# Kernel tuning notes

Measured on AMD Instinct MI355X. Metric: run time of the kernel, lower is better.

## Reference

```python
import jax, jax.numpy as jnp
import numpy as np

B, N, D = 4, 4096, 1024
DFF = 4 * D
K = 2048  # max(1, int(N * 0.5))


def setup_inputs() -> dict:
    key = jax.random.key(0)
    ks = jax.random.split(key, 4)
    x = jax.random.normal(ks[0], (B, N, D), dtype=jnp.float32)
    gate_w = jax.random.normal(ks[1], (1, D), dtype=jnp.float32) * 0.02
    w1 = jax.random.normal(ks[2], (D, DFF), dtype=jnp.float32) * (1.0 / np.sqrt(D))
    b1 = jnp.zeros((DFF,), dtype=jnp.float32)
    w2 = jax.random.normal(ks[3], (DFF, D), dtype=jnp.float32) * (1.0 / np.sqrt(DFF))
    b2 = jnp.zeros((D,), dtype=jnp.float32)
    return {"x": x, "gate_w": gate_w, "w1": w1, "b1": b1, "w2": w2, "b2": b2, "k": K}


def reference(x, gate_w, w1, b1, w2, b2, k):
    # scores: [B, N] = gate(x).squeeze(-1)
    scores = jnp.einsum("bnd,d->bn", x, gate_w[0])
    _, topk = jax.lax.top_k(scores, k)          # [B, k] token indices
    # gather selected tokens: [B, k, D]
    x_sel = jnp.take_along_axis(x, topk[:, :, None], axis=1)
    # ffn (d -> 4d -> d, GELU) + residual on selected tokens only
    h = jax.nn.gelu(x_sel @ w1 + b1) @ w2 + b2
    x_proc = x_sel + h
    # scatter processed tokens back into a copy of x
    b_idx = jnp.arange(x.shape[0])[:, None]      # [B, 1]
    out = x.at[b_idx, topk].set(x_proc)
    return out
```

## Files before the change

### kernel.cpp

```cpp
#include <hip/hip_runtime.h>
#include <math.h>

#define B_   4
#define N_   4096
#define D_   1024
#define DFF_ 4096
#define K_   2048

typedef __attribute__((ext_vector_type(8))) short short8;
typedef __attribute__((ext_vector_type(4))) float float4v;

__device__ __forceinline__ unsigned short f2bf(float f) {
    unsigned int u = __float_as_uint(f);
    u = (u + 0x7fffu + ((u >> 16) & 1u)) >> 16;
    return (unsigned short)u;
}

__device__ __forceinline__ void gld16(const void* g, void* l) {
    __builtin_amdgcn_global_load_lds((const __attribute__((address_space(1))) void*)g,
                                     (__attribute__((address_space(3))) void*)l, 16, 0, 0);
}

__global__ __launch_bounds__(256) void scores_kernel(const float* __restrict__ x,
                                                     const float* __restrict__ gate_w,
                                                     float* __restrict__ scores,
                                                     int* __restrict__ slot) {
    int wave = (blockIdx.x * blockDim.x + threadIdx.x) >> 6;
    int lane = threadIdx.x & 63;
    if (wave >= B_ * N_) return;
    if (lane == 1) slot[wave] = -1;
    const float4* xr = (const float4*)(x + (size_t)wave * D_);
    const float4* g  = (const float4*)gate_w;
    float acc = 0.f;
    #pragma unroll
    for (int j = 0; j < D_ / 4 / 64; ++j) {
        float4 a = xr[lane + j * 64];
        float4 b = g[lane + j * 64];
        acc += a.x * b.x + a.y * b.y + a.z * b.z + a.w * b.w;
    }
    #pragma unroll
    for (int off = 32; off > 0; off >>= 1) acc += __shfl_down(acc, off, 64);
    if (lane == 0) scores[wave] = acc;
}

__global__ __launch_bounds__(1024) void select_topk_kernel(const float* __restrict__ scores,
                                                           int* __restrict__ topk,
                                                           int* __restrict__ slot) {
    __shared__ unsigned key[N_];
    __shared__ unsigned hist[256];
    __shared__ int sh_bin, sh_rem, sh_ngt;
    __shared__ int wsum[16], woff[16];
    int b = blockIdx.x, tid = threadIdx.x;
    int lane = tid & 63, wid = tid >> 6;

    for (int i = tid; i < N_; i += 1024) {
        unsigned u = __float_as_uint(scores[b * N_ + i]);
        key[i] = (u & 0x80000000u) ? ~u : (u | 0x80000000u);
    }
    if (tid == 0) sh_ngt = 0;
    __syncthreads();

    unsigned prefix = 0, pmask = 0;
    int rem = K_;
    for (int shift = 24; shift >= 0; shift -= 8) {
        if (tid < 256) hist[tid] = 0;
        __syncthreads();
        for (int i = tid; i < N_; i += 1024) {
            unsigned k = key[i];
            if ((k & pmask) == prefix) atomicAdd(&hist[(k >> shift) & 255u], 1u);
        }
        __syncthreads();
        if (tid < 64) {
            unsigned v0 = hist[4 * lane], v1 = hist[4 * lane + 1];
            unsigned v2 = hist[4 * lane + 2], v3 = hist[4 * lane + 3];
            unsigned s3 = v3, s2 = v2 + s3, s1 = v1 + s2, s0 = v0 + s1;
            unsigned t = s0;
            #pragma unroll
            for (int off = 1; off < 64; off <<= 1) {
                unsigned u = __shfl_down(t, off, 64);
                if (lane + off < 64) t += u;
            }
            unsigned above = t - s0;
            unsigned S0 = s0 + above, S1 = s1 + above, S2 = s2 + above, S3 = s3 + above;
            unsigned R = (unsigned)rem;
            if (S0 >= R && S1 < R) { sh_bin = 4 * lane;     sh_rem = rem - (int)S1; }
            if (S1 >= R && S2 < R) { sh_bin = 4 * lane + 1; sh_rem = rem - (int)S2; }
            if (S2 >= R && S3 < R) { sh_bin = 4 * lane + 2; sh_rem = rem - (int)S3; }
            if (S3 >= R && above < R) { sh_bin = 4 * lane + 3; sh_rem = rem - (int)above; }
        }
        __syncthreads();
        prefix |= ((unsigned)sh_bin) << shift;
        pmask  |= 0xffu << shift;
        rem = sh_rem;
    }
    unsigned T = prefix;
    int c_gt = K_ - rem;

    for (int i = tid; i < N_; i += 1024) {
        bool p = key[i] > T;
        unsigned long long m = __ballot(p);
        int cnt = __popcll(m);
        int basepos = 0;
        if (lane == 0 && cnt) basepos = atomicAdd(&sh_ngt, cnt);
        basepos = __shfl(basepos, 0, 64);
        if (p) {
            int pos = basepos + __popcll(m & ((1ULL << lane) - 1ULL));
            topk[b * K_ + pos] = i;
            slot[b * N_ + i] = b * K_ + pos;
        }
    }
    int base = tid * 4, c = 0;
    #pragma unroll
    for (int j = 0; j < 4; ++j) c += (key[base + j] == T);
    int sc = c;
    #pragma unroll
    for (int off = 1; off < 64; off <<= 1) {
        int u = __shfl_up(sc, off, 64);
        if (lane >= off) sc += u;
    }
    if (lane == 63) wsum[wid] = sc;
    __syncthreads();
    if (tid == 0) {
        int run = 0;
        #pragma unroll
        for (int j = 0; j < 16; ++j) { woff[j] = run; run += wsum[j]; }
    }
    __syncthreads();
    int r = woff[wid] + sc - c;
    #pragma unroll
    for (int j = 0; j < 4; ++j) {
        if (key[base + j] == T) {
            if (r < rem) {
                topk[b * K_ + c_gt + r] = base + j;
                slot[b * N_ + base + j] = b * K_ + c_gt + r;
            }
            ++r;
        }
    }
}

__global__ __launch_bounds__(256) void gather_copy_kernel(const float* __restrict__ x,
                                                          const int* __restrict__ slot,
                                                          unsigned short* __restrict__ xsel,
                                                          float* __restrict__ out) {
    int row = blockIdx.x;
    int t = threadIdx.x;
    int s = slot[row];
    float4 v = ((const float4*)(x + (size_t)row * D_))[t];
    if (s >= 0) {
        ushort4 o;
        o.x = f2bf(v.x); o.y = f2bf(v.y); o.z = f2bf(v.z); o.w = f2bf(v.w);
        ((ushort4*)(xsel + (size_t)s * D_))[t] = o;
    } else {
        ((float4*)(out + (size_t)row * D_))[t] = v;
    }
}

__global__ __launch_bounds__(256) void transpose_both_kernel(const float* __restrict__ w1,
                                                             const float* __restrict__ w2,
                                                             unsigned short* __restrict__ w1t,
                                                             unsigned short* __restrict__ w2t) {
    __shared__ float tile[32][33];
    int bid = blockIdx.x;
    const float* src; unsigned short* dst; int R, C, bx, by;
    if (bid < 4096) { src = w1; dst = w1t; R = D_;   C = DFF_; bx = bid & 127;          by = bid >> 7; }
    else            { src = w2; dst = w2t; R = DFF_; C = D_;   bx = (bid - 4096) & 31;  by = (bid - 4096) >> 5; }
    int tx = threadIdx.x & 31, ty = threadIdx.x >> 5;
    int c = bx * 32 + tx, r0 = by * 32;
    #pragma unroll
    for (int j = ty; j < 32; j += 8) tile[j][tx] = src[(size_t)(r0 + j) * C + c];
    __syncthreads();
    int dc = by * 32 + tx, dr0 = bx * 32;
    #pragma unroll
    for (int j = ty; j < 32; j += 8) dst[(size_t)(dr0 + j) * R + dc] = f2bf(tile[tx][j]);
}


__global__ __launch_bounds__(512, 2) void ffn1_pipe_kernel(const unsigned short* __restrict__ A,
                                                           const unsigned short* __restrict__ Bt,
                                                           const float* __restrict__ b1,
                                                           unsigned short* __restrict__ h1) {
    constexpr int K  = D_;
    constexpr int NT = K / 32;
    __shared__ __align__(16) unsigned short smem[65536];

    const int t    = threadIdx.x;
    const int lane = t & 63;
    const int wid  = t >> 6;
    const int quad = lane >> 4;
    const int lr   = lane & 15;
    const int wr   = wid >> 2;
    const int wc   = wid & 3;
    const int row0 = blockIdx.x * 256;
    const int col0 = blockIdx.y * 256;

    const int ch0 = t, ch1 = t + 512;
    const int rp0 = ch0 >> 3, w0 = (ch0 & 7) ^ (rp0 & 7);
    const int rp1 = ch1 >> 3, w1 = (ch1 & 7) ^ (rp1 & 7);
    const int gr0 = rp0 * 2 + (w0 >> 2), gc0 = w0 & 3;
    const int gr1 = rp1 * 2 + (w1 >> 2), gc1 = w1 & 3;
    const char* aS0 = (const char*)A  + ((size_t)(row0 + gr0) * K + (size_t)gc0 * 8) * 2;
    const char* aS1 = (const char*)A  + ((size_t)(row0 + gr1) * K + (size_t)gc1 * 8) * 2;
    const char* bS0 = (const char*)Bt + ((size_t)(col0 + gr0) * K + (size_t)gc0 * 8) * 2;
    const char* bS1 = (const char*)Bt + ((size_t)(col0 + gr1) * K + (size_t)gc1 * 8) * 2;
    const int oA0 = ch0 * 8, oA1 = ch1 * 8;
    const int oB0 = 8192 + ch0 * 8, oB1 = 8192 + ch1 * 8;

    const int rbA = wr * 128 + lr, rA2 = rbA >> 1;
    const int aoff = (rA2 * 8 + ((((rbA & 1) << 2) | quad) ^ (rA2 & 7))) * 8;
    const int rbB = wc * 64 + lr, rB2 = rbB >> 1;
    const int boff = 8192 + (rB2 * 8 + ((((rbB & 1) << 2) | quad) ^ (rB2 & 7))) * 8;

    #pragma unroll
    for (int pt = 0; pt < 3; ++pt) {
        unsigned short* buf = smem + pt * 16384;
        gld16(aS0, buf + oA0); gld16(aS1, buf + oA1);
        gld16(bS0, buf + oB0); gld16(bS1, buf + oB1);
        aS0 += 64; aS1 += 64; bS0 += 64; bS1 += 64;
    }
    asm volatile("s_waitcnt vmcnt(8)" ::: "memory");
    __builtin_amdgcn_s_barrier();

    float4v acc[8][4] = {};
    short8 af[8], bq[4];

    #pragma unroll 4
    for (int kt = 0; kt < NT; ++kt) {
        unsigned short* cur = smem + (kt & 3) * 16384;
        unsigned short* nxt = smem + ((kt + 3) & 3) * 16384;
        const bool pf = (kt + 3 < NT);

        #pragma unroll
        for (int mi = 0; mi < 4; ++mi) af[mi] = *(const short8*)(cur + aoff + mi * 512);
        #pragma unroll
        for (int ni = 0; ni < 4; ++ni) bq[ni] = *(const short8*)(cur + boff + ni * 512);
        if (pf) { gld16(aS0, nxt + oA0); gld16(aS1, nxt + oA1); }
        __builtin_amdgcn_s_barrier();
        __builtin_amdgcn_s_setprio(1);
        #pragma unroll
        for (int mi = 0; mi < 4; ++mi)
            #pragma unroll
            for (int ni = 0; ni < 4; ++ni)
                acc[mi][ni] = __builtin_amdgcn_mfma_f32_16x16x32_bf16(af[mi], bq[ni], acc[mi][ni], 0, 0, 0);
        __builtin_amdgcn_s_setprio(0);
        __builtin_amdgcn_s_barrier();

        #pragma unroll
        for (int mi = 4; mi < 8; ++mi) af[mi] = *(const short8*)(cur + aoff + mi * 512);
        if (pf) { gld16(bS0, nxt + oB0); gld16(bS1, nxt + oB1); }
        aS0 += 64; aS1 += 64; bS0 += 64; bS1 += 64;
        if (kt < NT - 3)       asm volatile("s_waitcnt vmcnt(8)" ::: "memory");
        else if (kt == NT - 3) asm volatile("s_waitcnt vmcnt(4)" ::: "memory");
        else                   asm volatile("s_waitcnt vmcnt(0)" ::: "memory");
        __builtin_amdgcn_s_barrier();
        __builtin_amdgcn_s_setprio(1);
        #pragma unroll
        for (int mi = 4; mi < 8; ++mi)
            #pragma unroll
            for (int ni = 0; ni < 4; ++ni)
                acc[mi][ni] = __builtin_amdgcn_mfma_f32_16x16x32_bf16(af[mi], bq[ni], acc[mi][ni], 0, 0, 0);
        __builtin_amdgcn_s_setprio(0);
        __builtin_amdgcn_s_barrier();
    }

    float bias[4];
    #pragma unroll
    for (int ni = 0; ni < 4; ++ni) bias[ni] = b1[col0 + wc * 64 + ni * 16 + lr];
    unsigned short* ws_ = smem + wid * 5120;
    const int ro = row0 + wr * 128;
    const int co = col0 + wc * 64;
    #pragma unroll
    for (int p = 0; p < 2; ++p) {
        #pragma unroll
        for (int mi = 0; mi < 8; ++mi)
            #pragma unroll
            for (int nj = 0; nj < 2; ++nj) {
                const int ni = p * 2 + nj;
                #pragma unroll
                for (int r = 0; r < 4; ++r) {
                    float u = acc[mi][ni][r] + bias[ni];
                    float tt = 1.5957691216057308f * u * (1.0f + 0.044715f * u * u);
                    float g = u / (1.0f + __expf(-tt));
                    ws_[(mi * 16 + quad * 4 + r) * 40 + nj * 16 + lr] = f2bf(g);
                }
            }
        asm volatile("s_waitcnt lgkmcnt(0)" ::: "memory");
        #pragma unroll
        for (int j = 0; j < 8; ++j) {
            const int chk = lane + j * 64;
            const int rr = chk >> 2, cc = chk & 3;
            short8 v = *(const short8*)(ws_ + rr * 40 + cc * 8);
            *(short8*)(h1 + (size_t)(ro + rr) * DFF_ + co + p * 32 + cc * 8) = v;
        }
        asm volatile("s_waitcnt lgkmcnt(0)" ::: "memory");
    }
}

__global__ __launch_bounds__(512, 2) void ffn2_pipe_kernel(const unsigned short* __restrict__ A,
                                                           const unsigned short* __restrict__ Bt,
                                                           const float* __restrict__ b2,
                                                           const float* __restrict__ x,
                                                           const int* __restrict__ topk,
                                                           float* __restrict__ out) {
    constexpr int K  = DFF_;
    constexpr int NT = K / 32;
    __shared__ __align__(16) unsigned short smem[49152];

    const int t    = threadIdx.x;
    const int lane = t & 63;
    const int wid  = t >> 6;
    const int quad = lane >> 4;
    const int lr   = lane & 15;
    const int wr   = wid >> 2;
    const int wc   = wid & 3;
    const int row0 = blockIdx.x * 128;
    const int col0 = blockIdx.y * 256;

    const int chA = t;
    const int rpa = chA >> 3, wa = (chA & 7) ^ (rpa & 7);
    const char* aS = (const char*)A + ((size_t)(row0 + rpa * 2 + (wa >> 2)) * K + (size_t)(wa & 3) * 8) * 2;
    const int ch0 = t, ch1 = t + 512;
    const int rp0 = ch0 >> 3, w0 = (ch0 & 7) ^ (rp0 & 7);
    const int rp1 = ch1 >> 3, w1 = (ch1 & 7) ^ (rp1 & 7);
    const char* bS0 = (const char*)Bt + ((size_t)(col0 + rp0 * 2 + (w0 >> 2)) * K + (size_t)(w0 & 3) * 8) * 2;
    const char* bS1 = (const char*)Bt + ((size_t)(col0 + rp1 * 2 + (w1 >> 2)) * K + (size_t)(w1 & 3) * 8) * 2;
    const int oA = chA * 8;
    const int oB0 = 4096 + ch0 * 8, oB1 = 4096 + ch1 * 8;

    const int rbA = wr * 64 + lr, rA2 = rbA >> 1;
    const int aoff = (rA2 * 8 + ((((rbA & 1) << 2) | quad) ^ (rA2 & 7))) * 8;
    const int rbB = wc * 64 + lr, rB2 = rbB >> 1;
    const int boff = 4096 + (rB2 * 8 + ((((rbB & 1) << 2) | quad) ^ (rB2 & 7))) * 8;

    #pragma unroll
    for (int pt = 0; pt < 3; ++pt) {
        unsigned short* buf = smem + pt * 12288;
        gld16(aS, buf + oA); gld16(bS0, buf + oB0); gld16(bS1, buf + oB1);
        aS += 64; bS0 += 64; bS1 += 64;
    }
    asm volatile("s_waitcnt vmcnt(6)" ::: "memory");
    __builtin_amdgcn_s_barrier();

    float4v acc[4][4] = {};
    short8 af[4], bq[4];

    #pragma unroll 4
    for (int kt = 0; kt < NT; ++kt) {
        unsigned short* cur = smem + (kt & 3) * 12288;
        unsigned short* nxt = smem + ((kt + 3) & 3) * 12288;
        const bool pf = (kt + 3 < NT);

        af[0] = *(const short8*)(cur + aoff);
        af[1] = *(const short8*)(cur + aoff + 512);
        #pragma unroll
        for (int ni = 0; ni < 4; ++ni) bq[ni] = *(const short8*)(cur + boff + ni * 512);
        if (pf) { gld16(aS, nxt + oA); gld16(bS0, nxt + oB0); }
        __builtin_amdgcn_s_barrier();
        __builtin_amdgcn_s_setprio(1);
        #pragma unroll
        for (int mi = 0; mi < 2; ++mi)
            #pragma unroll
            for (int ni = 0; ni < 4; ++ni)
                acc[mi][ni] = __builtin_amdgcn_mfma_f32_16x16x32_bf16(af[mi], bq[ni], acc[mi][ni], 0, 0, 0);
        __builtin_amdgcn_s_setprio(0);
        __builtin_amdgcn_s_barrier();

        af[2] = *(const short8*)(cur + aoff + 1024);
        af[3] = *(const short8*)(cur + aoff + 1536);
        if (pf) { gld16(bS1, nxt + oB1); }
        aS += 64; bS0 += 64; bS1 += 64;
        if (kt < NT - 3)       asm volatile("s_waitcnt vmcnt(6)" ::: "memory");
        else if (kt == NT - 3) asm volatile("s_waitcnt vmcnt(3)" ::: "memory");
        else                   asm volatile("s_waitcnt vmcnt(0)" ::: "memory");
        __builtin_amdgcn_s_barrier();
        __builtin_amdgcn_s_setprio(1);
        #pragma unroll
        for (int mi = 2; mi < 4; ++mi)
            #pragma unroll
            for (int ni = 0; ni < 4; ++ni)
                acc[mi][ni] = __builtin_amdgcn_mfma_f32_16x16x32_bf16(af[mi], bq[ni], acc[mi][ni], 0, 0, 0);
        __builtin_amdgcn_s_setprio(0);
        __builtin_amdgcn_s_barrier();
    }

    #pragma unroll
    for (int mi = 0; mi < 4; ++mi) {
        #pragma unroll
        for (int r = 0; r < 4; ++r) {
            int row = row0 + wr * 64 + mi * 16 + quad * 4 + r;
            int gb = row >> 11;
            int tok = topk[row];
            size_t base = ((size_t)(gb * N_ + tok)) * D_;
            #pragma unroll
            for (int ni = 0; ni < 4; ++ni) {
                int col = col0 + wc * 64 + ni * 16 + lr;
                out[base + col] = x[base + col] + acc[mi][ni][r] + b2[col];
            }
        }
    }
}

extern "C" void kernel_launch(void* const* d_in, const int* in_sizes, int n_in,
                              void* d_out, int out_size, void* d_ws, size_t ws_size,
                              hipStream_t stream) {
    const float* x      = (const float*)d_in[0];
    const float* gate_w = (const float*)d_in[1];
    const float* w1     = (const float*)d_in[2];
    const float* b1     = (const float*)d_in[3];
    const float* w2     = (const float*)d_in[4];
    const float* b2     = (const float*)d_in[5];
    float* out = (float*)d_out;

    char* ws = (char*)d_ws;
    float*          scores = (float*)ws;
    int*            topk   = (int*)(ws + (64 << 10));
    int*            slot   = (int*)(ws + (96 << 10));
    unsigned short* xsel   = (unsigned short*)(ws + (160 << 10));
    unsigned short* w1t    = (unsigned short*)(ws + (160 << 10) + (16 << 20));
    unsigned short* w2t    = (unsigned short*)(ws + (160 << 10) + (24 << 20));
    unsigned short* h1     = (unsigned short*)(ws + (160 << 10) + (32 << 20));

    scores_kernel<<<(B_ * N_) / 4, 256, 0, stream>>>(x, gate_w, scores, slot);
    select_topk_kernel<<<B_, 1024, 0, stream>>>(scores, topk, slot);

    transpose_both_kernel<<<8192, 256, 0, stream>>>(w1, w2, w1t, w2t);

    gather_copy_kernel<<<B_ * N_, 256, 0, stream>>>(x, slot, xsel, out);

    ffn1_pipe_kernel<<<dim3(32, 16), 512, 0, stream>>>(xsel, w1t, b1, h1);
    ffn2_pipe_kernel<<<dim3(64, 4), 512, 0, stream>>>(h1, w2t, b2, x, topk, out);
}
```

Measured before the change: 335.4 us.

## Replace 4-stage LDS pipelines with smaller-tile double-buffered GEMM kernels

Both FFN GEMMs move from a 4-buffer, 3-deep prefetch pipeline with large block tiles to a simple two-buffer ping-pong scheme with smaller tiles. FFN1 goes from 256x256 to 256x128 tiles (more blocks, 4 blocks/CU bound), and FFN2 from 128x256 with 512 threads to 128x128 with 256 threads. The goal is higher occupancy and more blocks in flight, with less LDS per block, to hide latency. The cost is a full vmcnt(0) wait every k-step, which exposes global load latency, plus lower data reuse per tile.

```diff
diff --git a/kernel.cpp b/kernel.cpp
--- a/kernel.cpp
+++ b/kernel.cpp
@@ -176,66 +176,59 @@
 }
 
 
-__global__ __launch_bounds__(512, 2) void ffn1_pipe_kernel(const unsigned short* __restrict__ A,
-                                                           const unsigned short* __restrict__ Bt,
-                                                           const float* __restrict__ b1,
-                                                           unsigned short* __restrict__ h1) {
+__global__ __launch_bounds__(512, 4) void ffn1_db_kernel(const unsigned short* __restrict__ A,
+                                                         const unsigned short* __restrict__ Bt,
+                                                         const float* __restrict__ b1,
+                                                         unsigned short* __restrict__ h1) {
     constexpr int K  = D_;
     constexpr int NT = K / 32;
-    __shared__ __align__(16) unsigned short smem[65536];
+    __shared__ __align__(16) unsigned short smem[24576];
 
     const int t    = threadIdx.x;
     const int lane = t & 63;
     const int wid  = t >> 6;
     const int quad = lane >> 4;
     const int lr   = lane & 15;
-    const int wr   = wid >> 2;
-    const int wc   = wid & 3;
+    const int wr   = wid >> 1;
+    const int wc   = wid & 1;
     const int row0 = blockIdx.x * 256;
-    const int col0 = blockIdx.y * 256;
-
-    const int ch0 = t, ch1 = t + 512;
-    const int rp0 = ch0 >> 3, w0 = (ch0 & 7) ^ (rp0 & 7);
-    const int rp1 = ch1 >> 3, w1 = (ch1 & 7) ^ (rp1 & 7);
-    const int gr0 = rp0 * 2 + (w0 >> 2), gc0 = w0 & 3;
-    const int gr1 = rp1 * 2 + (w1 >> 2), gc1 = w1 & 3;
-    const char* aS0 = (const char*)A  + ((size_t)(row0 + gr0) * K + (size_t)gc0 * 8) * 2;
-    const char* aS1 = (const char*)A  + ((size_t)(row0 + gr1) * K + (size_t)gc1 * 8) * 2;
-    const char* bS0 = (const char*)Bt + ((size_t)(col0 + gr0) * K + (size_t)gc0 * 8) * 2;
-    const char* bS1 = (const char*)Bt + ((size_t)(col0 + gr1) * K + (size_t)gc1 * 8) * 2;
-    const int oA0 = ch0 * 8, oA1 = ch1 * 8;
-    const int oB0 = 8192 + ch0 * 8, oB1 = 8192 + ch1 * 8;
-
-    const int rbA = wr * 128 + lr, rA2 = rbA >> 1;
+    const int col0 = blockIdx.y * 128;
+
+    const int chA0 = t, chA1 = t + 512, chB = t;
+    const int rpA0 = chA0 >> 3, wA0 = (chA0 & 7) ^ (rpA0 & 7);
+    const int rpA1 = chA1 >> 3, wA1 = (chA1 & 7) ^ (rpA1 & 7);
+    const int rpB  = chB  >> 3, wB  = (chB  & 7) ^ (rpB  & 7);
+    const char* aS0 = (const char*)A  + ((size_t)(row0 + rpA0 * 2 + (wA0 >> 2)) * K + (size_t)(wA0 & 3) * 8) * 2;
+    const char* aS1 = (const char*)A  + ((size_t)(row0 + rpA1 * 2 + (wA1 >> 2)) * K + (size_t)(wA1 & 3) * 8) * 2;
+    const char* bS  = (const char*)Bt + ((size_t)(col0 + rpB  * 2 + (wB  >> 2)) * K + (size_t)(wB  & 3) * 8) * 2;
+    const int oA0 = chA0 * 8, oA1 = chA1 * 8, oB = 8192 + chB * 8;
+
+    const int rbA = wr * 64 + lr, rA2 = rbA >> 1;
     const int aoff = (rA2 * 8 + ((((rbA & 1) << 2) | quad) ^ (rA2 & 7))) * 8;
     const int rbB = wc * 64 + lr, rB2 = rbB >> 1;
     const int boff = 8192 + (rB2 * 8 + ((((rbB & 1) << 2) | quad) ^ (rB2 & 7))) * 8;
 
-    #pragma unroll
-    for (int pt = 0; pt < 3; ++pt) {
-        unsigned short* buf = smem + pt * 16384;
-        gld16(aS0, buf + oA0); gld16(aS1, buf + oA1);
-        gld16(bS0, buf + oB0); gld16(bS1, buf + oB1);
-        aS0 += 64; aS1 += 64; bS0 += 64; bS1 += 64;
-    }
-    asm volatile("s_waitcnt vmcnt(8)" ::: "memory");
+    unsigned short* lds0 = smem;
+    unsigned short* lds1 = smem + 12288;
+
+    gld16(aS0, lds0 + oA0); gld16(aS1, lds0 + oA1); gld16(bS, lds0 + oB);
+    aS0 += 64; aS1 += 64; bS += 64;
+    asm volatile("s_waitcnt vmcnt(0)" ::: "memory");
     __builtin_amdgcn_s_barrier();
 
-    float4v acc[8][4] = {};
-    short8 af[8], bq[4];
-
-    #pragma unroll 4
-    for (int kt = 0; kt < NT; ++kt) {
-        unsigned short* cur = smem + (kt & 3) * 16384;
-        unsigned short* nxt = smem + ((kt + 3) & 3) * 16384;
-        const bool pf = (kt + 3 < NT);
-
+    float4v acc[4][4] = {};
+    short8 af[4], bq[4];
+
+    auto step = [&](const unsigned short* cur, unsigned short* nxt, bool pf) {
         #pragma unroll
         for (int mi = 0; mi < 4; ++mi) af[mi] = *(const short8*)(cur + aoff + mi * 512);
         #pragma unroll
         for (int ni = 0; ni < 4; ++ni) bq[ni] = *(const short8*)(cur + boff + ni * 512);
-        if (pf) { gld16(aS0, nxt + oA0); gld16(aS1, nxt + oA1); }
-        __builtin_amdgcn_s_barrier();
+        if (pf) {
+            gld16(aS0, nxt + oA0); gld16(aS1, nxt + oA1); gld16(bS, nxt + oB);
+            aS0 += 64; aS1 += 64; bS += 64;
+        }
+        __builtin_amdgcn_sched_barrier(0);
         __builtin_amdgcn_s_setprio(1);
         #pragma unroll
         for (int mi = 0; mi < 4; ++mi)
@@ -243,88 +236,70 @@
             for (int ni = 0; ni < 4; ++ni)
                 acc[mi][ni] = __builtin_amdgcn_mfma_f32_16x16x32_bf16(af[mi], bq[ni], acc[mi][ni], 0, 0, 0);
         __builtin_amdgcn_s_setprio(0);
+        asm volatile("s_waitcnt vmcnt(0)" ::: "memory");
         __builtin_amdgcn_s_barrier();
-
-        #pragma unroll
-        for (int mi = 4; mi < 8; ++mi) af[mi] = *(const short8*)(cur + aoff + mi * 512);
-        if (pf) { gld16(bS0, nxt + oB0); gld16(bS1, nxt + oB1); }
-        aS0 += 64; aS1 += 64; bS0 += 64; bS1 += 64;
-        if (kt < NT - 3)       asm volatile("s_waitcnt vmcnt(8)" ::: "memory");
-        else if (kt == NT - 3) asm volatile("s_waitcnt vmcnt(4)" ::: "memory");
-        else                   asm volatile("s_waitcnt vmcnt(0)" ::: "memory");
-        __builtin_amdgcn_s_barrier();
-        __builtin_amdgcn_s_setprio(1);
-        #pragma unroll
-        for (int mi = 4; mi < 8; ++mi)
-            #pragma unroll
-            for (int ni = 0; ni < 4; ++ni)
-                acc[mi][ni] = __builtin_amdgcn_mfma_f32_16x16x32_bf16(af[mi], bq[ni], acc[mi][ni], 0, 0, 0);
-        __builtin_amdgcn_s_setprio(0);
-        __builtin_amdgcn_s_barrier();
-    }
+    };
+
+    for (int kt = 0; kt < NT - 2; kt += 2) { step(lds0, lds1, true); step(lds1, lds0, true); }
+    step(lds0, lds1, true);
+    step(lds1, lds0, false);
 
     float bias[4];
     #pragma unroll
     for (int ni = 0; ni < 4; ++ni) bias[ni] = b1[col0 + wc * 64 + ni * 16 + lr];
-    unsigned short* ws_ = smem + wid * 5120;
-    const int ro = row0 + wr * 128;
-    const int co = col0 + wc * 64;
-    #pragma unroll
-    for (int p = 0; p < 2; ++p) {
-        #pragma unroll
-        for (int mi = 0; mi < 8; ++mi)
-            #pragma unroll
-            for (int nj = 0; nj < 2; ++nj) {
-                const int ni = p * 2 + nj;
-                #pragma unroll
-                for (int r = 0; r < 4; ++r) {
-                    float u = acc[mi][ni][r] + bias[ni];
-                    float tt = 1.5957691216057308f * u * (1.0f + 0.044715f * u * u);
-                    float g = u / (1.0f + __expf(-tt));
-                    ws_[(mi * 16 + quad * 4 + r) * 40 + nj * 16 + lr] = f2bf(g);
-                }
+    unsigned short* ws_ = smem + wid * 1056;
+    const int ro = row0 + wr * 64, co = col0 + wc * 64;
+    #pragma unroll
+    for (int mi = 0; mi < 4; ++mi) {
+        #pragma unroll
+        for (int ni = 0; ni < 4; ++ni)
+            #pragma unroll
+            for (int r = 0; r < 4; ++r) {
+                float u = acc[mi][ni][r] + bias[ni];
+                float tt = 1.5957691216057308f * u * (1.0f + 0.044715f * u * u);
+                float g = u / (1.0f + __expf(-tt));
+                ws_[(quad * 4 + r) * 66 + ni * 16 + lr] = f2bf(g);
             }
         asm volatile("s_waitcnt lgkmcnt(0)" ::: "memory");
         #pragma unroll
-        for (int j = 0; j < 8; ++j) {
-            const int chk = lane + j * 64;
-            const int rr = chk >> 2, cc = chk & 3;
-            short8 v = *(const short8*)(ws_ + rr * 40 + cc * 8);
-            *(short8*)(h1 + (size_t)(ro + rr) * DFF_ + co + p * 32 + cc * 8) = v;
+        for (int j = 0; j < 2; ++j) {
+            int chk = lane + j * 64;
+            int rr = chk >> 3, cc = chk & 7;
+            *(short8*)(h1 + (size_t)(ro + mi * 16 + rr) * DFF_ + co + cc * 8) =
+                *(const short8*)(ws_ + rr * 66 + cc * 8);
         }
         asm volatile("s_waitcnt lgkmcnt(0)" ::: "memory");
     }
 }
 
-__global__ __launch_bounds__(512, 2) void ffn2_pipe_kernel(const unsigned short* __restrict__ A,
-                                                           const unsigned short* __restrict__ Bt,
-                                                           const float* __restrict__ b2,
-                                                           const float* __restrict__ x,
-                                                           const int* __restrict__ topk,
-                                                           float* __restrict__ out) {
+__global__ __launch_bounds__(256, 2) void ffn2_db_kernel(const unsigned short* __restrict__ A,
+                                                         const unsigned short* __restrict__ Bt,
+                                                         const float* __restrict__ b2,
+                                                         const float* __restrict__ x,
+                                                         const int* __restrict__ topk,
+                                                         float* __restrict__ out) {
     constexpr int K  = DFF_;
     constexpr int NT = K / 32;
-    __shared__ __align__(16) unsigned short smem[49152];
+    __shared__ __align__(16) unsigned short smem[16384];
 
     const int t    = threadIdx.x;
     const int lane = t & 63;
     const int wid  = t >> 6;
     const int quad = lane >> 4;
     const int lr   = lane & 15;
-    const int wr   = wid >> 2;
-    const int wc   = wid & 3;
+    const int wr   = wid >> 1;
+    const int wc   = wid & 1;
     const int row0 = blockIdx.x * 128;
-    const int col0 = blockIdx.y * 256;
-
-    const int chA = t;
-    const int rpa = chA >> 3, wa = (chA & 7) ^ (rpa & 7);
-    const char* aS = (const char*)A + ((size_t)(row0 + rpa * 2 + (wa >> 2)) * K + (size_t)(wa & 3) * 8) * 2;
-    const int ch0 = t, ch1 = t + 512;
+    const int col0 = blockIdx.y * 128;
+
+    const int ch0 = t, ch1 = t + 256;
     const int rp0 = ch0 >> 3, w0 = (ch0 & 7) ^ (rp0 & 7);
     const int rp1 = ch1 >> 3, w1 = (ch1 & 7) ^ (rp1 & 7);
+    const char* aS0 = (const char*)A  + ((size_t)(row0 + rp0 * 2 + (w0 >> 2)) * K + (size_t)(w0 & 3) * 8) * 2;
+    const char* aS1 = (const char*)A  + ((size_t)(row0 + rp1 * 2 + (w1 >> 2)) * K + (size_t)(w1 & 3) * 8) * 2;
     const char* bS0 = (const char*)Bt + ((size_t)(col0 + rp0 * 2 + (w0 >> 2)) * K + (size_t)(w0 & 3) * 8) * 2;
     const char* bS1 = (const char*)Bt + ((size_t)(col0 + rp1 * 2 + (w1 >> 2)) * K + (size_t)(w1 & 3) * 8) * 2;
-    const int oA = chA * 8;
+    const int oA0 = ch0 * 8, oA1 = ch1 * 8;
     const int oB0 = 4096 + ch0 * 8, oB1 = 4096 + ch1 * 8;
 
     const int rbA = wr * 64 + lr, rA2 = rbA >> 1;
@@ -332,56 +307,43 @@
     const int rbB = wc * 64 + lr, rB2 = rbB >> 1;
     const int boff = 4096 + (rB2 * 8 + ((((rbB & 1) << 2) | quad) ^ (rB2 & 7))) * 8;
 
-    #pragma unroll
-    for (int pt = 0; pt < 3; ++pt) {
-        unsigned short* buf = smem + pt * 12288;
-        gld16(aS, buf + oA); gld16(bS0, buf + oB0); gld16(bS1, buf + oB1);
-        aS += 64; bS0 += 64; bS1 += 64;
-    }
-    asm volatile("s_waitcnt vmcnt(6)" ::: "memory");
+    unsigned short* lds0 = smem;
+    unsigned short* lds1 = smem + 8192;
+
+    gld16(aS0, lds0 + oA0); gld16(aS1, lds0 + oA1);
+    gld16(bS0, lds0 + oB0); gld16(bS1, lds0 + oB1);
+    aS0 += 64; aS1 += 64; bS0 += 64; bS1 += 64;
+    asm volatile("s_waitcnt vmcnt(0)" ::: "memory");
     __builtin_amdgcn_s_barrier();
 
     float4v acc[4][4] = {};
     short8 af[4], bq[4];
 
-    #pragma unroll 4
-    for (int kt = 0; kt < NT; ++kt) {
-        unsigned short* cur = smem + (kt & 3) * 12288;
-        unsigned short* nxt = smem + ((kt + 3) & 3) * 12288;
-        const bool pf = (kt + 3 < NT);
-
-        af[0] = *(const short8*)(cur + aoff);
-        af[1] = *(const short8*)(cur + aoff + 512);
+    auto step = [&](const unsigned short* cur, unsigned short* nxt, bool pf) {
+        #pragma unroll
+        for (int mi = 0; mi < 4; ++mi) af[mi] = *(const short8*)(cur + aoff + mi * 512);
         #pragma unroll
         for (int ni = 0; ni < 4; ++ni) bq[ni] = *(const short8*)(cur + boff + ni * 512);
-        if (pf) { gld16(aS, nxt + oA); gld16(bS0, nxt + oB0); }
-        __builtin_amdgcn_s_barrier();
+        if (pf) {
+            gld16(aS0, nxt + oA0); gld16(aS1, nxt + oA1);
+            gld16(bS0, nxt + oB0); gld16(bS1, nxt + oB1);
+            aS0 += 64; aS1 += 64; bS0 += 64; bS1 += 64;
+        }
+        __builtin_amdgcn_sched_barrier(0);
         __builtin_amdgcn_s_setprio(1);
         #pragma unroll
-        for (int mi = 0; mi < 2; ++mi)
+        for (int mi = 0; mi < 4; ++mi)
             #pragma unroll
             for (int ni = 0; ni < 4; ++ni)
                 acc[mi][ni] = __builtin_amdgcn_mfma_f32_16x16x32_bf16(af[mi], bq[ni], acc[mi][ni], 0, 0, 0);
         __builtin_amdgcn_s_setprio(0);
+        asm volatile("s_waitcnt vmcnt(0)" ::: "memory");
         __builtin_amdgcn_s_barrier();
-
-        af[2] = *(const short8*)(cur + aoff + 1024);
-        af[3] = *(const short8*)(cur + aoff + 1536);
-        if (pf) { gld16(bS1, nxt + oB1); }
-        aS += 64; bS0 += 64; bS1 += 64;
-        if (kt < NT - 3)       asm volatile("s_waitcnt vmcnt(6)" ::: "memory");
-        else if (kt == NT - 3) asm volatile("s_waitcnt vmcnt(3)" ::: "memory");
-        else                   asm volatile("s_waitcnt vmcnt(0)" ::: "memory");
-        __builtin_amdgcn_s_barrier();
-        __builtin_amdgcn_s_setprio(1);
-        #pragma unroll
-        for (int mi = 2; mi < 4; ++mi)
-            #pragma unroll
-            for (int ni = 0; ni < 4; ++ni)
-                acc[mi][ni] = __builtin_amdgcn_mfma_f32_16x16x32_bf16(af[mi], bq[ni], acc[mi][ni], 0, 0, 0);
-        __builtin_amdgcn_s_setprio(0);
-        __builtin_amdgcn_s_barrier();
-    }
+    };
+
+    for (int kt = 0; kt < NT - 2; kt += 2) { step(lds0, lds1, true); step(lds1, lds0, true); }
+    step(lds0, lds1, true);
+    step(lds1, lds0, false);
 
     #pragma unroll
     for (int mi = 0; mi < 4; ++mi) {
@@ -427,6 +389,6 @@
 
     gather_copy_kernel<<<B_ * N_, 256, 0, stream>>>(x, slot, xsel, out);
 
-    ffn1_pipe_kernel<<<dim3(32, 16), 512, 0, stream>>>(xsel, w1t, b1, h1);
-    ffn2_pipe_kernel<<<dim3(64, 4), 512, 0, stream>>>(h1, w2t, b2, x, topk, out);
-}
+    ffn1_db_kernel<<<dim3(32, 32), 512, 0, stream>>>(xsel, w1t, b1, h1);
+    ffn2_db_kernel<<<dim3(64, 8), 256, 0, stream>>>(h1, w2t, b2, x, topk, out);
+}
```

New measurement: 329.8 us. Within noise of the previous version (-1.7%).
